# Kernel tuning notes

Hardware: AMD Instinct MI355X
Metric: run time of the kernel (lower is better)

The kernel has to match this reference:

```python
import math
import jax, jax.numpy as jnp
import numpy as np

B, C, DM, H = 4, 2048, 128, 8  # batch, after_reduced_cnn_size (seq), d_model, heads
DPH = DM // H                  # 16
K = 7                          # causal conv kernel size


def _causal_conv1d(x, w, b):
    # x: (B, C, L); w: (C_out, C_in, K); left-pad by K-1 -> causal, 'same' length
    xp = jnp.pad(x, ((0, 0), (0, 0), (w.shape[-1] - 1, 0)))
    y = jax.lax.conv_general_dilated(xp, w, (1,), 'VALID',
                                     dimension_numbers=('NCH', 'OIH', 'NCH'))
    return y + b[None, :, None]


def _split_heads(x):
    # (B, S, H*DPH) layout after view: (B, C, DM) -> (B, H, C, DPH)
    return x.reshape(x.shape[0], -1, H, DPH).transpose(0, 2, 1, 3)


def setup_inputs() -> dict:
    rng = jax.random.key(0)
    ks = jax.random.split(rng, 9)
    conv_scale = 1.0 / math.sqrt(C * K)
    lin_scale = 1.0 / math.sqrt(DM)
    return {
        'query': jax.random.normal(ks[0], (B, C, DM), dtype=jnp.float32),
        'key': jax.random.normal(ks[1], (B, C, DM), dtype=jnp.float32),
        'value': jax.random.normal(ks[2], (B, C, DM), dtype=jnp.float32),
        'conv_k_w': jax.random.normal(ks[3], (C, C, K), dtype=jnp.float32) * conv_scale,
        'conv_k_b': jnp.zeros((C,), dtype=jnp.float32),
        'conv_v_w': jax.random.normal(ks[4], (C, C, K), dtype=jnp.float32) * conv_scale,
        'conv_v_b': jnp.zeros((C,), dtype=jnp.float32),
        'lin_w': jax.random.normal(ks[5], (DM, DM), dtype=jnp.float32) * lin_scale,
        'lin_b': jnp.zeros((DM,), dtype=jnp.float32),
    }


def reference(query, key, value, conv_k_w, conv_k_b, conv_v_w, conv_v_b, lin_w, lin_b):
    # query used as-is; key/value pass through causal convs (convs[1], convs[2])
    q = _split_heads(query)                                   # (B,H,C,DPH)
    k = _split_heads(_causal_conv1d(key, conv_k_w, conv_k_b))  # (B,H,C,DPH)
    v = _split_heads(_causal_conv1d(value, conv_v_w, conv_v_b))
    scores = jnp.einsum('bhqd,bhkd->bhqk', q, k) / math.sqrt(DPH)
    p = jax.nn.softmax(scores, axis=-1)                       # (B,H,C,C)
    x = jnp.einsum('bhqk,bhkd->bhqd', p, v)                   # dropout p=0 => same as x_raw
    x = x.transpose(0, 2, 1, 3).reshape(x.shape[0], -1, H * DPH)
    return x @ lin_w.T + lin_b
```

## Files before the change

### kernel.cpp

```cpp
#include <hip/hip_runtime.h>
#include <cstdint>
#include <cstddef>

#define B_   4
#define C_   2048
#define DM_  128
#define H_   8
#define KK_  14336
#define N_   512

#define KSPLIT 8
#define KPB   1792
#define NITER 56
#define YSZ   ((size_t)B_ * C_ * DM_)

typedef unsigned short u16;
typedef __attribute__((ext_vector_type(8))) short  s16x8;
typedef __attribute__((ext_vector_type(4))) float  f32x4;

typedef const __attribute__((address_space(1))) void gvoid;
typedef __attribute__((address_space(3))) void lvoid;

__device__ __forceinline__ void gl2lds16(const void* g, void* l) {
    __builtin_amdgcn_global_load_lds((gvoid*)g, (lvoid*)l, 16, 0, 0);
}

__device__ __forceinline__ void gload4(float4& d, const float* p) {
    asm volatile("global_load_dwordx4 %0, %1, off" : "=v"(d) : "v"(p) : "memory");
}

__device__ __forceinline__ u16 f2bf(float f) {
    uint32_t u = __builtin_bit_cast(uint32_t, f);
    u += 0x7fffu + ((u >> 16) & 1u);
    return (u16)(u >> 16);
}
__device__ __forceinline__ uint32_t pk2(float a, float b) {
    return (uint32_t)f2bf(a) | ((uint32_t)f2bf(b) << 16);
}

__global__ __launch_bounds__(256) void prep_bimt(const float* __restrict__ key,
                                                 const float* __restrict__ value,
                                                 u16* __restrict__ bk,
                                                 u16* __restrict__ bv) {
    const float* src = blockIdx.z ? value : key;
    u16*         dst = blockIdx.z ? bv : bk;
    int gid = blockIdx.x * 256 + threadIdx.x;
    int cp = gid & 1023;
    int n  = gid >> 10;
    int b = n >> 7, l = n & 127;
    const float* s0 = src + (size_t)(b * C_ + cp * 2) * DM_;
    u16 hh[14];
#pragma unroll
    for (int r = 0; r < 2; ++r) {
#pragma unroll
        for (int t = 0; t < 7; ++t) {
            int j = l + t - 6;
            float v = (j >= 0) ? s0[r * DM_ + j] : 0.0f;
            hh[r * 7 + t] = f2bf(v);
        }
    }
    uint32_t* D = (uint32_t*)dst + (size_t)n * (KK_ / 2) + cp * 7;
#pragma unroll
    for (int i = 0; i < 7; ++i)
        D[i] = (uint32_t)hh[2 * i] | ((uint32_t)hh[2 * i + 1] << 16);
}

__global__ __launch_bounds__(256) void prep_q(const float4* __restrict__ q, uint2* __restrict__ qb) {
    int i = blockIdx.x * 256 + threadIdx.x;
    float4 v = q[i];
    uint2 r;
    r.x = pk2(v.x * 0.25f, v.y * 0.25f);
    r.y = pk2(v.z * 0.25f, v.w * 0.25f);
    qb[i] = r;
}

__global__ __launch_bounds__(256, 2) void conv_gemm(
        const float* __restrict__ Wk, const float* __restrict__ Wv,
        const u16* __restrict__ Bk, const u16* __restrict__ Bv,
        float* __restrict__ Ypk, float* __restrict__ Ypv) {
    const int conv = blockIdx.z >> 3;
    const int sk   = blockIdx.z & 7;
    const float* W  = conv ? Wv : Wk;
    const u16*   Bm = conv ? Bv : Bk;
    float*       Yp = (conv ? Ypv : Ypk) + (size_t)sk * YSZ;
    const int m0 = blockIdx.x * 128;
    const int n0 = blockIdx.y * 256;
    const int kbeg = sk * KPB;

    __shared__ __align__(16) u16 Al[2][128 * 32];
    __shared__ __align__(16) u16 Bl[3][256 * 32];

    const int tid = threadIdx.x;
    const int wave = tid >> 6, lane = tid & 63;
    const int l16 = lane & 15, quad = lane >> 4;
    const int wm = wave >> 1, wn = wave & 1;

    const int arow = tid >> 1, ahalf = tid & 1;
    const float* wp = W + (size_t)(m0 + arow) * KK_ + kbeg + ahalf * 16;
    const int asw = (arow >> 1) & 3;
    const int aoff0 = arow * 32 + (((ahalf * 2)     ^ asw) * 8);
    const int aoff1 = arow * 32 + (((ahalf * 2 + 1) ^ asw) * 8);

    const u16* bgp[4];
    int boff[4];
    {
        const int br = lane >> 2, bs = lane & 3;
#pragma unroll
        for (int p = 0; p < 4; ++p) {
            int row = wave * 64 + p * 16 + br;
            int gc = (bs ^ ((row >> 1) & 3)) * 8;
            bgp[p] = Bm + (size_t)(n0 + row) * KK_ + kbeg + gc;
            boff[p] = (wave * 64 + p * 16) * 32;
        }
    }

    f32x4 acc[4][8];
#pragma unroll
    for (int i = 0; i < 4; ++i)
#pragma unroll
        for (int j = 0; j < 8; ++j) acc[i][j] = (f32x4){0.f, 0.f, 0.f, 0.f};

    float4 wr0, wr1, wr2, wr3;
    {
#pragma unroll
        for (int p = 0; p < 4; ++p)
            gl2lds16(bgp[p], &Bl[0][boff[p]]);
        float4 a0, a1, a2, a3;
        gload4(a0, wp);      gload4(a1, wp + 4);
        gload4(a2, wp + 8);  gload4(a3, wp + 12);
#pragma unroll
        for (int p = 0; p < 4; ++p)
            gl2lds16(bgp[p] + 32, &Bl[1][boff[p]]);
        gload4(wr0, wp + 32); gload4(wr1, wp + 36);
        gload4(wr2, wp + 40); gload4(wr3, wp + 44);
        asm volatile("s_waitcnt vmcnt(8)" ::: "memory");
        __builtin_amdgcn_sched_barrier(0);
        uint4 p0, p1;
        p0.x = pk2(a0.x, a0.y); p0.y = pk2(a0.z, a0.w);
        p0.z = pk2(a1.x, a1.y); p0.w = pk2(a1.z, a1.w);
        p1.x = pk2(a2.x, a2.y); p1.y = pk2(a2.z, a2.w);
        p1.z = pk2(a3.x, a3.y); p1.w = pk2(a3.z, a3.w);
        *(uint4*)&Al[0][aoff0] = p0;
        *(uint4*)&Al[0][aoff1] = p1;
        asm volatile("s_waitcnt lgkmcnt(0)" ::: "memory");
        __builtin_amdgcn_sched_barrier(0);
        __builtin_amdgcn_s_barrier();
    }

    int bcur = 0;
    for (int t = 0; t < NITER; ++t) {
        const int ap = t & 1;
        int bst = bcur - 1; if (bst < 0) bst = 2;
        const int kb = (t + 2 < NITER) ? t + 2 : NITER - 1;

        s16x8 af[4];
#pragma unroll
        for (int fm = 0; fm < 4; ++fm) {
            int r = wm * 64 + fm * 16 + l16;
            af[fm] = *(const s16x8*)&Al[ap][r * 32 + ((quad ^ ((r >> 1) & 3)) * 8)];
        }
        s16x8 bfr[4];
#pragma unroll
        for (int fn = 0; fn < 4; ++fn) {
            int n = wn * 128 + fn * 16 + l16;
            bfr[fn] = *(const s16x8*)&Bl[bcur][n * 32 + ((quad ^ ((n >> 1) & 3)) * 8)];
        }
#pragma unroll
        for (int p = 0; p < 4; ++p)
            gl2lds16(bgp[p] + (size_t)kb * 32, &Bl[bst][boff[p]]);
#pragma unroll
        for (int fm = 0; fm < 4; ++fm)
#pragma unroll
            for (int fn = 0; fn < 4; ++fn)
                acc[fm][fn] = __builtin_amdgcn_mfma_f32_16x16x32_bf16(af[fm], bfr[fn], acc[fm][fn], 0, 0, 0);
#pragma unroll
        for (int fn = 0; fn < 4; ++fn) {
            int n = wn * 128 + (fn + 4) * 16 + l16;
            bfr[fn] = *(const s16x8*)&Bl[bcur][n * 32 + ((quad ^ ((n >> 1) & 3)) * 8)];
        }
#pragma unroll
        for (int fm = 0; fm < 4; ++fm)
#pragma unroll
            for (int fn = 0; fn < 4; ++fn)
                acc[fm][fn + 4] = __builtin_amdgcn_mfma_f32_16x16x32_bf16(af[fm], bfr[fn], acc[fm][fn + 4], 0, 0, 0);

        asm volatile("s_waitcnt vmcnt(4)" ::: "memory");
        __builtin_amdgcn_sched_barrier(0);

        {
            uint4 q0, q1;
            q0.x = pk2(wr0.x, wr0.y); q0.y = pk2(wr0.z, wr0.w);
            q0.z = pk2(wr1.x, wr1.y); q0.w = pk2(wr1.z, wr1.w);
            q1.x = pk2(wr2.x, wr2.y); q1.y = pk2(wr2.z, wr2.w);
            q1.z = pk2(wr3.x, wr3.y); q1.w = pk2(wr3.z, wr3.w);
            *(uint4*)&Al[ap ^ 1][aoff0] = q0;
            *(uint4*)&Al[ap ^ 1][aoff1] = q1;
        }
        gload4(wr0, wp + (size_t)kb * 32);
        gload4(wr1, wp + (size_t)kb * 32 + 4);
        gload4(wr2, wp + (size_t)kb * 32 + 8);
        gload4(wr3, wp + (size_t)kb * 32 + 12);

        asm volatile("s_waitcnt lgkmcnt(0)" ::: "memory");
        __builtin_amdgcn_sched_barrier(0);
        __builtin_amdgcn_s_barrier();

        bcur = (bcur == 2) ? 0 : bcur + 1;
    }
    asm volatile("s_waitcnt vmcnt(0)" ::: "memory");
    __builtin_amdgcn_sched_barrier(0);

#pragma unroll
    for (int fm = 0; fm < 4; ++fm) {
        int m = m0 + wm * 64 + fm * 16 + quad * 4;
#pragma unroll
        for (int fn = 0; fn < 8; ++fn) {
            int n = n0 + wn * 128 + fn * 16 + l16;
            int bb = n >> 7, ll = n & 127;
            float* yp = Yp + ((size_t)(bb * C_ + m)) * DM_ + ll;
#pragma unroll
            for (int r = 0; r < 4; ++r)
                yp[(size_t)r * DM_] = acc[fm][fn][r];
        }
    }
}

__global__ __launch_bounds__(256) void kv_prep(
        const float* __restrict__ Ypk, const float* __restrict__ Ypv,
        const float* __restrict__ bkb, const float* __restrict__ bvb,
        u16* __restrict__ Kbf, u16* __restrict__ Vbf) {
    int gid = blockIdx.x * 256 + threadIdx.x;
    int key = gid & 2047;
    int bh  = gid >> 11;
    int b = bh >> 3, h = bh & 7;
    size_t src = ((size_t)(b * C_ + key)) * DM_ + h * 16;
    float kb = bkb[key], vb = bvb[key];

    float ka[16] = {0.f, 0.f, 0.f, 0.f, 0.f, 0.f, 0.f, 0.f,
                    0.f, 0.f, 0.f, 0.f, 0.f, 0.f, 0.f, 0.f};
    float va[16] = {0.f, 0.f, 0.f, 0.f, 0.f, 0.f, 0.f, 0.f,
                    0.f, 0.f, 0.f, 0.f, 0.f, 0.f, 0.f, 0.f};
#pragma unroll
    for (int sk = 0; sk < KSPLIT; ++sk) {
        const float* pk = Ypk + (size_t)sk * YSZ + src;
        const float* pv = Ypv + (size_t)sk * YSZ + src;
#pragma unroll
        for (int c = 0; c < 4; ++c) {
            float4 fk = *(const float4*)(pk + c * 4);
            float4 fv = *(const float4*)(pv + c * 4);
            ka[c * 4 + 0] += fk.x; ka[c * 4 + 1] += fk.y;
            ka[c * 4 + 2] += fk.z; ka[c * 4 + 3] += fk.w;
            va[c * 4 + 0] += fv.x; va[c * 4 + 1] += fv.y;
            va[c * 4 + 2] += fv.z; va[c * 4 + 3] += fv.w;
        }
    }

    uint4 pA, pB;
    pA.x = pk2(ka[0] + kb, ka[1] + kb);  pA.y = pk2(ka[2] + kb, ka[3] + kb);
    pA.z = pk2(ka[4] + kb, ka[5] + kb);  pA.w = pk2(ka[6] + kb, ka[7] + kb);
    pB.x = pk2(ka[8] + kb, ka[9] + kb);  pB.y = pk2(ka[10] + kb, ka[11] + kb);
    pB.z = pk2(ka[12] + kb, ka[13] + kb); pB.w = pk2(ka[14] + kb, ka[15] + kb);
    u16* kd = Kbf + ((size_t)bh * C_ + key) * 16;
    *(uint4*)kd       = pA;
    *(uint4*)(kd + 8) = pB;

    u16* vdst = Vbf + (size_t)bh * 16 * C_ + key;
#pragma unroll
    for (int d = 0; d < 16; ++d)
        vdst[(size_t)d * C_] = f2bf(va[d] + vb);
}

__global__ __launch_bounds__(256, 4) void attn_k(
        const u16* __restrict__ Kbf, const u16* __restrict__ Vbf,
        const u16* __restrict__ qb, u16* __restrict__ att) {
    const int q0 = blockIdx.x * 64;
    const int bh = blockIdx.y;
    const int b = bh >> 3, h = bh & 7;

    __shared__ __align__(16) u16 Kl[128 * 24];
    __shared__ __align__(16) u16 Vl[16 * 128];
    __shared__ __align__(16) u16 Pl[64 * 136];

    const int tid = threadIdx.x;
    const int wave = tid >> 6, lane = tid & 63;
    const int l16 = lane & 15, quad = lane >> 4;
    const float LOG2E = 1.44269504088896340736f;

    const u16* kgp = Kbf + ((size_t)bh * C_ + (tid >> 1)) * 16 + (tid & 1) * 8;
    u16* kld = &Kl[(tid >> 1) * 24 + (tid & 1) * 8];
    const int vd = wave * 4 + (lane >> 4);
    const u16* vgp = Vbf + ((size_t)bh * 16 + vd) * C_ + (size_t)(((lane & 15) ^ (vd & 7)) * 8);
    u16* vld = &Vl[wave * 4 * 128];

    s16x8 qf = {};
    if (quad < 2) {
        const u16* qp = qb + ((size_t)(b * C_ + q0 + wave * 16 + l16)) * DM_ + h * 16 + quad * 8;
        qf = *(const s16x8*)qp;
    }
    f32x4 o = (f32x4){0.f, 0.f, 0.f, 0.f};
    float mr[4] = {-3e38f, -3e38f, -3e38f, -3e38f};
    float lr[4] = {0.f, 0.f, 0.f, 0.f};

    for (int kt = 0; kt < 16; ++kt) {
        const int k0 = kt * 128;
        __syncthreads();
        {
            uint4 kv = *(const uint4*)(kgp + (size_t)k0 * 16);
            *(uint4*)kld = kv;
            gl2lds16(vgp + k0, vld);
        }
        __syncthreads();

        f32x4 sf[8];
#pragma unroll
        for (int fn = 0; fn < 8; ++fn) {
            s16x8 kb = {};
            if (quad < 2) kb = *(const s16x8*)&Kl[(fn * 16 + l16) * 24 + quad * 8];
            sf[fn] = __builtin_amdgcn_mfma_f32_16x16x32_bf16(qf, kb, (f32x4){0.f, 0.f, 0.f, 0.f}, 0, 0, 0);
        }

        float mt[4];
#pragma unroll
        for (int r = 0; r < 4; ++r) {
            float m = sf[0][r];
#pragma unroll
            for (int fn = 1; fn < 8; ++fn) m = fmaxf(m, sf[fn][r]);
            m = fmaxf(m, __shfl_xor(m, 1));
            m = fmaxf(m, __shfl_xor(m, 2));
            m = fmaxf(m, __shfl_xor(m, 4));
            m = fmaxf(m, __shfl_xor(m, 8));
            mt[r] = m;
        }
        float al[4], ps[4];
#pragma unroll
        for (int r = 0; r < 4; ++r) {
            float mnew = fmaxf(mr[r], mt[r]);
            al[r] = exp2f((mr[r] - mnew) * LOG2E);
            mr[r] = mnew;
            ps[r] = 0.f;
        }
#pragma unroll
        for (int fn = 0; fn < 8; ++fn) {
#pragma unroll
            for (int r = 0; r < 4; ++r) {
                float p = exp2f((sf[fn][r] - mr[r]) * LOG2E);
                ps[r] += p;
                Pl[(wave * 16 + quad * 4 + r) * 136 + fn * 16 + l16] = f2bf(p);
            }
        }
#pragma unroll
        for (int r = 0; r < 4; ++r) {
            float t = ps[r];
            t += __shfl_xor(t, 1);
            t += __shfl_xor(t, 2);
            t += __shfl_xor(t, 4);
            t += __shfl_xor(t, 8);
            lr[r] = lr[r] * al[r] + t;
            o[r] *= al[r];
        }
#pragma unroll
        for (int ko = 0; ko < 4; ++ko) {
            s16x8 pa = *(const s16x8*)&Pl[(wave * 16 + l16) * 136 + ko * 32 + quad * 8];
            s16x8 vb = *(const s16x8*)&Vl[l16 * 128 + (((ko * 4 + quad) ^ (l16 & 7)) * 8)];
            o = __builtin_amdgcn_mfma_f32_16x16x32_bf16(pa, vb, o, 0, 0, 0);
        }
    }

#pragma unroll
    for (int r = 0; r < 4; ++r) {
        float inv = 1.0f / lr[r];
        int row = q0 + wave * 16 + quad * 4 + r;
        att[((size_t)(b * C_ + row)) * DM_ + h * 16 + l16] = f2bf(o[r] * inv);
    }
}

__global__ __launch_bounds__(256, 2) void lin_k(
        const u16* __restrict__ att, const float* __restrict__ lw,
        const float* __restrict__ lb, float* __restrict__ out) {
    const int r0 = blockIdx.x * 32;
    __shared__ __align__(16) u16 Wl[128 * 136];
    __shared__ __align__(16) u16 Atl[32 * 136];
    const int tid = threadIdx.x;
    const int wave = tid >> 6, lane = tid & 63;
    const int l16 = lane & 15, quad = lane >> 4;

    {
        int j = tid >> 1, half = tid & 1;
        const float* src = lw + (size_t)j * DM_ + half * 64;
        u16* dstp = &Wl[j * 136 + half * 64];
#pragma unroll
        for (int c = 0; c < 8; ++c) {
            float4 f0 = *(const float4*)(src + c * 8);
            float4 f1 = *(const float4*)(src + c * 8 + 4);
            uint4 p;
            p.x = pk2(f0.x, f0.y); p.y = pk2(f0.z, f0.w);
            p.z = pk2(f1.x, f1.y); p.w = pk2(f1.z, f1.w);
            *(uint4*)(dstp + c * 8) = p;
        }
    }
    {
        int row = tid >> 3, seg = tid & 7;
        const uint4* src = (const uint4*)(att + ((size_t)(r0 + row)) * DM_ + seg * 16);
        uint4 a0 = src[0], a1 = src[1];
        *(uint4*)&Atl[row * 136 + seg * 16]     = a0;
        *(uint4*)&Atl[row * 136 + seg * 16 + 8] = a1;
    }
    __syncthreads();

    const int wn0 = wave * 32;
    f32x4 acc[2][2];
#pragma unroll
    for (int i = 0; i < 2; ++i)
#pragma unroll
        for (int j = 0; j < 2; ++j) acc[i][j] = (f32x4){0.f, 0.f, 0.f, 0.f};
#pragma unroll
    for (int ko = 0; ko < 4; ++ko) {
        s16x8 af[2], bf[2];
#pragma unroll
        for (int fm = 0; fm < 2; ++fm)
            af[fm] = *(const s16x8*)&Atl[(fm * 16 + l16) * 136 + ko * 32 + quad * 8];
#pragma unroll
        for (int fn = 0; fn < 2; ++fn)
            bf[fn] = *(const s16x8*)&Wl[(wn0 + fn * 16 + l16) * 136 + ko * 32 + quad * 8];
#pragma unroll
        for (int fm = 0; fm < 2; ++fm)
#pragma unroll
            for (int fn = 0; fn < 2; ++fn)
                acc[fm][fn] = __builtin_amdgcn_mfma_f32_16x16x32_bf16(af[fm], bf[fn], acc[fm][fn], 0, 0, 0);
    }
#pragma unroll
    for (int fm = 0; fm < 2; ++fm) {
#pragma unroll
        for (int fn = 0; fn < 2; ++fn) {
            int col = wn0 + fn * 16 + l16;
            float bias = lb[col];
#pragma unroll
            for (int r = 0; r < 4; ++r) {
                int row = r0 + fm * 16 + quad * 4 + r;
                out[(size_t)row * DM_ + col] = acc[fm][fn][r] + bias;
            }
        }
    }
}

extern "C" void kernel_launch(void* const* d_in, const int* in_sizes, int n_in,
                              void* d_out, int out_size, void* d_ws, size_t ws_size,
                              hipStream_t stream) {
    const float* query = (const float*)d_in[0];
    const float* key   = (const float*)d_in[1];
    const float* value = (const float*)d_in[2];
    const float* wk    = (const float*)d_in[3];
    const float* bk    = (const float*)d_in[4];
    const float* wv    = (const float*)d_in[5];
    const float* bv    = (const float*)d_in[6];
    const float* lw    = (const float*)d_in[7];
    const float* lb    = (const float*)d_in[8];
    float* out = (float*)d_out;

    char* ws = (char*)d_ws;
    u16*   bimt_k = (u16*)(ws);
    u16*   bimt_v = (u16*)(ws + 14680064);
    u16*   qbf    = (u16*)(ws + 29360128);
    u16*   att    = (u16*)(ws + 31457280);
    u16*   kbf    = (u16*)(ws + 33554432);
    u16*   vbf    = (u16*)(ws + 35651584);
    float* ypk    = (float*)(ws + 37748736);
    float* ypv    = (float*)(ws + 71303168);

    prep_bimt<<<dim3(2048, 1, 2), 256, 0, stream>>>(key, value, bimt_k, bimt_v);
    prep_q<<<1024, 256, 0, stream>>>((const float4*)query, (uint2*)qbf);
    conv_gemm<<<dim3(16, 2, 16), 256, 0, stream>>>(wk, wv, bimt_k, bimt_v, ypk, ypv);
    kv_prep<<<256, 256, 0, stream>>>(ypk, ypv, bk, bv, kbf, vbf);
    attn_k<<<dim3(32, 32), 256, 0, stream>>>(kbf, vbf, qbf, att);
    lin_k<<<256, 256, 0, stream>>>(att, lw, lb, out);
}
```

Measured before the change: 470.4 us.

## Double-buffer K/V tiles in attention, coalesce kv_prep reads, use raw v_exp

The attention kernel now double-buffers its K and V LDS tiles. It prefetches the next tile's global loads while the current tile is computed, which cuts the loop to one barrier per iteration. kv_prep is remapped so 32 lanes read one contiguous 128-float row, giving coalesced split-K reduction reads across four times as many blocks, at the cost of scattered 2-byte V stores. exp2f is replaced by an inline v_exp_f32, dropping the range-handling code at some accuracy cost for extreme inputs. The extra LDS per block may lower occupancy.

```diff
diff --git a/kernel.cpp b/kernel.cpp
--- a/kernel.cpp
+++ b/kernel.cpp
@@ -27,6 +27,12 @@
 
 __device__ __forceinline__ void gload4(float4& d, const float* p) {
     asm volatile("global_load_dwordx4 %0, %1, off" : "=v"(d) : "v"(p) : "memory");
+}
+
+__device__ __forceinline__ float fexp2(float x) {
+    float r;
+    asm("v_exp_f32 %0, %1" : "=v"(r) : "v"(x));
+    return r;
 }
 
 __device__ __forceinline__ u16 f2bf(float f) {
@@ -229,45 +235,35 @@
         const float* __restrict__ Ypk, const float* __restrict__ Ypv,
         const float* __restrict__ bkb, const float* __restrict__ bvb,
         u16* __restrict__ Kbf, u16* __restrict__ Vbf) {
-    int gid = blockIdx.x * 256 + threadIdx.x;
-    int key = gid & 2047;
-    int bh  = gid >> 11;
-    int b = bh >> 3, h = bh & 7;
-    size_t src = ((size_t)(b * C_ + key)) * DM_ + h * 16;
-    float kb = bkb[key], vb = bvb[key];
-
-    float ka[16] = {0.f, 0.f, 0.f, 0.f, 0.f, 0.f, 0.f, 0.f,
-                    0.f, 0.f, 0.f, 0.f, 0.f, 0.f, 0.f, 0.f};
-    float va[16] = {0.f, 0.f, 0.f, 0.f, 0.f, 0.f, 0.f, 0.f,
-                    0.f, 0.f, 0.f, 0.f, 0.f, 0.f, 0.f, 0.f};
+    const int tid = threadIdx.x;
+    const int rid = blockIdx.x * 8 + (tid >> 5);
+    const int lane32 = tid & 31;
+    const int b = rid >> 11, key = rid & 2047;
+    const int d0 = lane32 * 4;
+    const size_t src = (size_t)rid * DM_ + d0;
+
+    float kx = 0.f, ky = 0.f, kz = 0.f, kw = 0.f;
+    float vx = 0.f, vy = 0.f, vz = 0.f, vw = 0.f;
 #pragma unroll
     for (int sk = 0; sk < KSPLIT; ++sk) {
-        const float* pk = Ypk + (size_t)sk * YSZ + src;
-        const float* pv = Ypv + (size_t)sk * YSZ + src;
-#pragma unroll
-        for (int c = 0; c < 4; ++c) {
-            float4 fk = *(const float4*)(pk + c * 4);
-            float4 fv = *(const float4*)(pv + c * 4);
-            ka[c * 4 + 0] += fk.x; ka[c * 4 + 1] += fk.y;
-            ka[c * 4 + 2] += fk.z; ka[c * 4 + 3] += fk.w;
-            va[c * 4 + 0] += fv.x; va[c * 4 + 1] += fv.y;
-            va[c * 4 + 2] += fv.z; va[c * 4 + 3] += fv.w;
-        }
-    }
-
-    uint4 pA, pB;
-    pA.x = pk2(ka[0] + kb, ka[1] + kb);  pA.y = pk2(ka[2] + kb, ka[3] + kb);
-    pA.z = pk2(ka[4] + kb, ka[5] + kb);  pA.w = pk2(ka[6] + kb, ka[7] + kb);
-    pB.x = pk2(ka[8] + kb, ka[9] + kb);  pB.y = pk2(ka[10] + kb, ka[11] + kb);
-    pB.z = pk2(ka[12] + kb, ka[13] + kb); pB.w = pk2(ka[14] + kb, ka[15] + kb);
-    u16* kd = Kbf + ((size_t)bh * C_ + key) * 16;
-    *(uint4*)kd       = pA;
-    *(uint4*)(kd + 8) = pB;
-
-    u16* vdst = Vbf + (size_t)bh * 16 * C_ + key;
-#pragma unroll
-    for (int d = 0; d < 16; ++d)
-        vdst[(size_t)d * C_] = f2bf(va[d] + vb);
+        float4 fk = *(const float4*)(Ypk + (size_t)sk * YSZ + src);
+        float4 fv = *(const float4*)(Ypv + (size_t)sk * YSZ + src);
+        kx += fk.x; ky += fk.y; kz += fk.z; kw += fk.w;
+        vx += fv.x; vy += fv.y; vz += fv.z; vw += fv.w;
+    }
+    const float kb = bkb[key], vb = bvb[key];
+
+    const int h = d0 >> 4, dd = d0 & 15;
+    uint2 kp;
+    kp.x = pk2(kx + kb, ky + kb);
+    kp.y = pk2(kz + kb, kw + kb);
+    *(uint2*)(Kbf + (((size_t)(b * 8 + h) * C_ + key) * 16 + dd)) = kp;
+
+    u16* vd = Vbf + ((size_t)(b * 8 + h) * 16 + dd) * C_ + key;
+    vd[0]          = f2bf(vx + vb);
+    vd[(size_t)C_]     = f2bf(vy + vb);
+    vd[(size_t)C_ * 2] = f2bf(vz + vb);
+    vd[(size_t)C_ * 3] = f2bf(vw + vb);
 }
 
 __global__ __launch_bounds__(256, 4) void attn_k(
@@ -277,8 +273,8 @@
     const int bh = blockIdx.y;
     const int b = bh >> 3, h = bh & 7;
 
-    __shared__ __align__(16) u16 Kl[128 * 24];
-    __shared__ __align__(16) u16 Vl[16 * 128];
+    __shared__ __align__(16) u16 Kl[2][128 * 24];
+    __shared__ __align__(16) u16 Vl[2][16 * 128];
     __shared__ __align__(16) u16 Pl[64 * 136];
 
     const int tid = threadIdx.x;
@@ -287,10 +283,10 @@
     const float LOG2E = 1.44269504088896340736f;
 
     const u16* kgp = Kbf + ((size_t)bh * C_ + (tid >> 1)) * 16 + (tid & 1) * 8;
-    u16* kld = &Kl[(tid >> 1) * 24 + (tid & 1) * 8];
+    const int kofs = (tid >> 1) * 24 + (tid & 1) * 8;
     const int vd = wave * 4 + (lane >> 4);
     const u16* vgp = Vbf + ((size_t)bh * 16 + vd) * C_ + (size_t)(((lane & 15) ^ (vd & 7)) * 8);
-    u16* vld = &Vl[wave * 4 * 128];
+    const int vofs = wave * 4 * 128;
 
     s16x8 qf = {};
     if (quad < 2) {
@@ -301,21 +297,27 @@
     float mr[4] = {-3e38f, -3e38f, -3e38f, -3e38f};
     float lr[4] = {0.f, 0.f, 0.f, 0.f};
 
+    {
+        uint4 kv = *(const uint4*)(kgp);
+        *(uint4*)&Kl[0][kofs] = kv;
+        gl2lds16(vgp, &Vl[0][vofs]);
+    }
+    __syncthreads();
+
     for (int kt = 0; kt < 16; ++kt) {
-        const int k0 = kt * 128;
-        __syncthreads();
-        {
-            uint4 kv = *(const uint4*)(kgp + (size_t)k0 * 16);
-            *(uint4*)kld = kv;
-            gl2lds16(vgp + k0, vld);
-        }
-        __syncthreads();
+        const int cur = kt & 1;
+        const bool pre = (kt < 15);
+        uint4 kvn = {};
+        if (pre) {
+            kvn = *(const uint4*)(kgp + (size_t)(kt + 1) * 128 * 16);
+            gl2lds16(vgp + (size_t)(kt + 1) * 128, &Vl[cur ^ 1][vofs]);
+        }
 
         f32x4 sf[8];
 #pragma unroll
         for (int fn = 0; fn < 8; ++fn) {
             s16x8 kb = {};
-            if (quad < 2) kb = *(const s16x8*)&Kl[(fn * 16 + l16) * 24 + quad * 8];
+            if (quad < 2) kb = *(const s16x8*)&Kl[cur][(fn * 16 + l16) * 24 + quad * 8];
             sf[fn] = __builtin_amdgcn_mfma_f32_16x16x32_bf16(qf, kb, (f32x4){0.f, 0.f, 0.f, 0.f}, 0, 0, 0);
         }
 
@@ -335,7 +337,7 @@
 #pragma unroll
         for (int r = 0; r < 4; ++r) {
             float mnew = fmaxf(mr[r], mt[r]);
-            al[r] = exp2f((mr[r] - mnew) * LOG2E);
+            al[r] = fexp2((mr[r] - mnew) * LOG2E);
             mr[r] = mnew;
             ps[r] = 0.f;
         }
@@ -343,11 +345,12 @@
         for (int fn = 0; fn < 8; ++fn) {
 #pragma unroll
             for (int r = 0; r < 4; ++r) {
-                float p = exp2f((sf[fn][r] - mr[r]) * LOG2E);
+                float p = fexp2((sf[fn][r] - mr[r]) * LOG2E);
                 ps[r] += p;
                 Pl[(wave * 16 + quad * 4 + r) * 136 + fn * 16 + l16] = f2bf(p);
             }
         }
+        if (pre) *(uint4*)&Kl[cur ^ 1][kofs] = kvn;
 #pragma unroll
         for (int r = 0; r < 4; ++r) {
             float t = ps[r];
@@ -361,9 +364,10 @@
 #pragma unroll
         for (int ko = 0; ko < 4; ++ko) {
             s16x8 pa = *(const s16x8*)&Pl[(wave * 16 + l16) * 136 + ko * 32 + quad * 8];
-            s16x8 vb = *(const s16x8*)&Vl[l16 * 128 + (((ko * 4 + quad) ^ (l16 & 7)) * 8)];
+            s16x8 vb = *(const s16x8*)&Vl[cur][l16 * 128 + (((ko * 4 + quad) ^ (l16 & 7)) * 8)];
             o = __builtin_amdgcn_mfma_f32_16x16x32_bf16(pa, vb, o, 0, 0, 0);
         }
+        __syncthreads();
     }
 
 #pragma unroll
@@ -470,7 +474,7 @@
     prep_bimt<<<dim3(2048, 1, 2), 256, 0, stream>>>(key, value, bimt_k, bimt_v);
     prep_q<<<1024, 256, 0, stream>>>((const float4*)query, (uint2*)qbf);
     conv_gemm<<<dim3(16, 2, 16), 256, 0, stream>>>(wk, wv, bimt_k, bimt_v, ypk, ypv);
-    kv_prep<<<256, 256, 0, stream>>>(ypk, ypv, bk, bv, kbf, vbf);
+    kv_prep<<<1024, 256, 0, stream>>>(ypk, ypv, bk, bv, kbf, vbf);
     attn_k<<<dim3(32, 32), 256, 0, stream>>>(kbf, vbf, qbf, att);
     lin_k<<<256, 256, 0, stream>>>(att, lw, lb, out);
 }
```

After: 453.0 us. 3.7% less time.
